# Optimization experiments

Hardware: AMD Instinct MI355X
Metric: run time of the kernel (lower is better)

The kernel has to match this reference:

```python
import jax, jax.numpy as jnp
import numpy as np
from jax.experimental.ode import odeint

DT = 0.01  # matches init kwarg dt


def setup_inputs() -> dict:
    key = jax.random.key(0)
    kx, kw = jax.random.split(key)
    B, D, T = 8192, 128, 64
    x = jax.random.normal(kx, (B, D), dtype=jnp.float32)
    # nnx.Linear kernel (in_features, out_features), lecun-normal-like scale
    W = jax.random.normal(kw, (D, D), dtype=jnp.float32) / np.float32(np.sqrt(D))
    return {"x": x, "W": W, "T": T}


def reference(x, W, T):
    # dynamics_fn(z, t) = Linear(z) = z @ W  (no bias), time-invariant linear ODE
    time_points = DT * jnp.arange(1, T + 1, dtype=jnp.float32)  # dt*[1..T]
    # odeint: y0 = x is the state at time_points[0]; preds: (T, B, D)
    preds = odeint(lambda z, t: z @ W, x, time_points)
    return jnp.transpose(preds, (1, 0, 2))  # (B, T, D)
```

## Files before the change

kernel.cpp:

```cpp
#include <hip/hip_runtime.h>
#include <stdint.h>

#define DD   128
#define TT   64
#define BB   8192
#define NPOW 8

typedef float  f32x4  __attribute__((ext_vector_type(4)));
typedef __bf16 bf16x8 __attribute__((ext_vector_type(8)));

__device__ __forceinline__ unsigned short f2bf(float f) {
  unsigned u = __builtin_bit_cast(unsigned, f);
  u += 0x7fffu + ((u >> 16) & 1u);
  return (unsigned short)(u >> 16);
}

__global__ void cvt_x_kernel(const float* __restrict__ x, unsigned short* __restrict__ xb) {
  int i = (blockIdx.x * 256 + threadIdx.x) * 4;
  float4 v = *(const float4*)(x + i);
  unsigned long long u =  (unsigned long long)f2bf(v.x)
                       | ((unsigned long long)f2bf(v.y) << 16)
                       | ((unsigned long long)f2bf(v.z) << 32)
                       | ((unsigned long long)f2bf(v.w) << 48);
  *(unsigned long long*)(xb + i) = u;
}

__global__ void transpose_kernel(const float* __restrict__ W, float* __restrict__ Wt) {
  __shared__ float t[32][33];
  int bx = blockIdx.x & 3, by = blockIdx.x >> 2;
  int r = threadIdx.x >> 3;
  int c = (threadIdx.x & 7) * 4;
  float4 v = *(const float4*)(W + (by * 32 + r) * DD + bx * 32 + c);
  t[r][c] = v.x; t[r][c + 1] = v.y; t[r][c + 2] = v.z; t[r][c + 3] = v.w;
  __syncthreads();
  float4 o = { t[c + 0][r], t[c + 1][r], t[c + 2][r], t[c + 3][r] };
  *(float4*)(Wt + (bx * 32 + r) * DD + by * 32 + c) = o;
}

__global__ __launch_bounds__(256) void powmm_kernel(float* __restrict__ Wp,
                                                    int aPow, int bBase, int dstBase) {
  int mat = blockIdx.x >> 4;
  int rb  = blockIdx.x & 15;
  const float* A = Wp + (aPow - 1) * DD * DD;
  const float* B = Wp + (bBase + mat - 1) * DD * DD;
  float* C = Wp + (dstBase + mat - 1) * DD * DD;

  __shared__ float Bs[DD * DD];
  __shared__ float As[8 * DD];
  for (int i = threadIdx.x; i < DD * DD / 4; i += 256)
    ((float4*)Bs)[i] = ((const float4*)B)[i];
  for (int i = threadIdx.x; i < 8 * DD / 4; i += 256)
    ((float4*)As)[i] = ((const float4*)(A + rb * 8 * DD))[i];
  __syncthreads();

  int r  = threadIdx.x >> 5;
  int c0 = (threadIdx.x & 31) * 4;
  f32x4 acc = {0.f, 0.f, 0.f, 0.f};
  for (int k = 0; k < DD; ++k) {
    float a = As[r * DD + k];
    f32x4 b = *(const f32x4*)(Bs + k * DD + c0);
    acc += a * b;
  }
  *(f32x4*)(C + (rb * 8 + r) * DD + c0) = acc;
}

__global__ __launch_bounds__(256) void combine_kernel(const float* __restrict__ Wp,
                                                      unsigned short* __restrict__ Pb) {
  int j    = blockIdx.x >> 4;
  int part = blockIdx.x & 15;
  float c[NPOW];
  double t = (double)j * 0.01, cc = 1.0;
  for (int n = 1; n <= NPOW; ++n) { cc *= t / (double)n; c[n - 1] = (float)cc; }

  int e0 = part * 1024 + threadIdx.x * 4;
  f32x4 acc;
#pragma unroll
  for (int i = 0; i < 4; ++i) {
    int e = e0 + i;
    acc[i] = ((e >> 7) == (e & 127)) ? 1.0f : 0.0f;
  }
#pragma unroll
  for (int n = 0; n < NPOW; ++n) {
    f32x4 w = *(const f32x4*)(Wp + n * DD * DD + e0);
    acc += c[n] * w;
  }
  unsigned long long u =  (unsigned long long)f2bf(acc[0])
                       | ((unsigned long long)f2bf(acc[1]) << 16)
                       | ((unsigned long long)f2bf(acc[2]) << 32)
                       | ((unsigned long long)f2bf(acc[3]) << 48);
  *(unsigned long long*)(Pb + j * DD * DD + e0) = u;
}

__global__ __launch_bounds__(256, 4) void gemm_kernel(
    const unsigned short* __restrict__ xb,
    const unsigned short* __restrict__ Pb,
    float* __restrict__ out) {
  const int n    = blockIdx.x;
  const int bt   = n >> 6;
  const int jo   = n & 63;
  const int j    = ((jo & 7) << 3) | (jo >> 3);
  const int tid  = threadIdx.x;
  const int w    = tid >> 6;
  const int l    = tid & 63;
  const int quad = l >> 4;
  const int li   = l & 15;

  const int mq = (w >> 1) * 64;
  const int nq = (w & 1) * 64;

  const unsigned short* gA = xb + bt * DD * DD;
  const unsigned short* gB = Pb + j * DD * DD;

  f32x4 acc[4][4];
#pragma unroll
  for (int mt = 0; mt < 4; ++mt)
#pragma unroll
    for (int nt = 0; nt < 4; ++nt) acc[mt][nt] = (f32x4){0.f, 0.f, 0.f, 0.f};

#pragma unroll
  for (int ks = 0; ks < 4; ++ks) {
    bf16x8 af[4], bf[4];
#pragma unroll
    for (int mt = 0; mt < 4; ++mt)
      af[mt] = *(const bf16x8*)(gA + (mq + mt * 16 + li) * DD + ks * 32 + quad * 8);
#pragma unroll
    for (int nt = 0; nt < 4; ++nt)
      bf[nt] = *(const bf16x8*)(gB + (nq + nt * 16 + li) * DD + ks * 32 + quad * 8);
#pragma unroll
    for (int mt = 0; mt < 4; ++mt)
#pragma unroll
      for (int nt = 0; nt < 4; ++nt)
        acc[mt][nt] = __builtin_amdgcn_mfma_f32_16x16x32_bf16(bf[nt], af[mt], acc[mt][nt], 0, 0, 0);
  }

  const size_t orow = (size_t)(TT * DD);
  float* obase = out + (size_t)(bt * DD) * orow + j * DD;
#pragma unroll
  for (int mt = 0; mt < 4; ++mt) {
    float* orow_p = obase + (size_t)(mq + mt * 16 + li) * orow + quad * 4;
#pragma unroll
    for (int nt = 0; nt < 4; ++nt)
      *(f32x4*)(orow_p + nq + nt * 16) = acc[mt][nt];
  }
}

extern "C" void kernel_launch(void* const* d_in, const int* in_sizes, int n_in,
                              void* d_out, int out_size, void* d_ws, size_t ws_size,
                              hipStream_t stream) {
  const float* x = (const float*)d_in[0];
  const float* W = (const float*)d_in[1];
  float* out = (float*)d_out;

  float* Wp = (float*)d_ws;
  unsigned short* Pb = (unsigned short*)((char*)d_ws + NPOW * DD * DD * sizeof(float));
  unsigned short* xb = Pb + TT * DD * DD;

  cvt_x_kernel<<<BB * DD / (256 * 4), 256, 0, stream>>>(x, xb);
  transpose_kernel<<<16, 256, 0, stream>>>(W, Wp);

  powmm_kernel<<<16, 256, 0, stream>>>(Wp, 1, 1, 2);
  powmm_kernel<<<32, 256, 0, stream>>>(Wp, 2, 1, 3);
  powmm_kernel<<<64, 256, 0, stream>>>(Wp, 4, 1, 5);

  combine_kernel<<<TT * 16, 256, 0, stream>>>(Wp, Pb);

  gemm_kernel<<<4096, 256, 0, stream>>>(xb, Pb, out);
}
```

Baseline: 327.4 us.

## Restructure GEMM so each block owns 16 rows and loops over all time steps

The output GEMM now launches one block per 16 batch rows instead of one block per (128-row tile, time step) pair. The block keeps its A fragments in registers and loops serially over all 64 propagator matrices, each wave computing a 16x32 output slice per step. The goal is to load x only once and write every output row contiguously across time. In exchange each block does much less MFMA work per load, re-reads all B matrices from L2 per block, and the serial j loop lowers parallelism and latency hiding.

```diff
diff --git a/kernel.cpp b/kernel.cpp
--- a/kernel.cpp
+++ b/kernel.cpp
@@ -91,56 +91,41 @@
   *(unsigned long long*)(Pb + j * DD * DD + e0) = u;
 }
 
-__global__ __launch_bounds__(256, 4) void gemm_kernel(
+__global__ __launch_bounds__(256) void gemm_kernel(
     const unsigned short* __restrict__ xb,
     const unsigned short* __restrict__ Pb,
     float* __restrict__ out) {
-  const int n    = blockIdx.x;
-  const int bt   = n >> 6;
-  const int jo   = n & 63;
-  const int j    = ((jo & 7) << 3) | (jo >> 3);
+  const int bt   = blockIdx.x;
   const int tid  = threadIdx.x;
   const int w    = tid >> 6;
   const int l    = tid & 63;
   const int quad = l >> 4;
   const int li   = l & 15;
+  const int nq   = w * 32;
 
-  const int mq = (w >> 1) * 64;
-  const int nq = (w & 1) * 64;
-
-  const unsigned short* gA = xb + bt * DD * DD;
-  const unsigned short* gB = Pb + j * DD * DD;
-
-  f32x4 acc[4][4];
+  const unsigned short* gA = xb + (size_t)(bt * 16) * DD;
+  bf16x8 af[4];
 #pragma unroll
-  for (int mt = 0; mt < 4; ++mt)
-#pragma unroll
-    for (int nt = 0; nt < 4; ++nt) acc[mt][nt] = (f32x4){0.f, 0.f, 0.f, 0.f};
-
-#pragma unroll
-  for (int ks = 0; ks < 4; ++ks) {
-    bf16x8 af[4], bf[4];
-#pragma unroll
-    for (int mt = 0; mt < 4; ++mt)
-      af[mt] = *(const bf16x8*)(gA + (mq + mt * 16 + li) * DD + ks * 32 + quad * 8);
-#pragma unroll
-    for (int nt = 0; nt < 4; ++nt)
-      bf[nt] = *(const bf16x8*)(gB + (nq + nt * 16 + li) * DD + ks * 32 + quad * 8);
-#pragma unroll
-    for (int mt = 0; mt < 4; ++mt)
-#pragma unroll
-      for (int nt = 0; nt < 4; ++nt)
-        acc[mt][nt] = __builtin_amdgcn_mfma_f32_16x16x32_bf16(bf[nt], af[mt], acc[mt][nt], 0, 0, 0);
-  }
+  for (int ks = 0; ks < 4; ++ks)
+    af[ks] = *(const bf16x8*)(gA + li * DD + ks * 32 + quad * 8);
 
   const size_t orow = (size_t)(TT * DD);
-  float* obase = out + (size_t)(bt * DD) * orow + j * DD;
+  float* orow_p = out + (size_t)(bt * 16 + li) * orow + nq + quad * 4;
+
+#pragma unroll 1
+  for (int j = 0; j < TT; ++j) {
+    const unsigned short* gB = Pb + j * DD * DD;
+    f32x4 acc0 = {0.f, 0.f, 0.f, 0.f};
+    f32x4 acc1 = {0.f, 0.f, 0.f, 0.f};
 #pragma unroll
-  for (int mt = 0; mt < 4; ++mt) {
-    float* orow_p = obase + (size_t)(mq + mt * 16 + li) * orow + quad * 4;
-#pragma unroll
-    for (int nt = 0; nt < 4; ++nt)
-      *(f32x4*)(orow_p + nq + nt * 16) = acc[mt][nt];
+    for (int ks = 0; ks < 4; ++ks) {
+      bf16x8 bf0 = *(const bf16x8*)(gB + (nq +  0 + li) * DD + ks * 32 + quad * 8);
+      bf16x8 bf1 = *(const bf16x8*)(gB + (nq + 16 + li) * DD + ks * 32 + quad * 8);
+      acc0 = __builtin_amdgcn_mfma_f32_16x16x32_bf16(bf0, af[ks], acc0, 0, 0, 0);
+      acc1 = __builtin_amdgcn_mfma_f32_16x16x32_bf16(bf1, af[ks], acc1, 0, 0, 0);
+    }
+    *(f32x4*)(orow_p + j * DD)      = acc0;
+    *(f32x4*)(orow_p + j * DD + 16) = acc1;
   }
 }
 
@@ -164,5 +149,5 @@
 
   combine_kernel<<<TT * 16, 256, 0, stream>>>(Wp, Pb);
 
-  gemm_kernel<<<4096, 256, 0, stream>>>(xb, Pb, out);
+  gemm_kernel<<<BB / 16, 256, 0, stream>>>(xb, Pb, out);
 }
```

After: 377.0 us. 15.1% more time.
